# Kernel optimization log

Measured on AMD Instinct MI355X. Metric: run time of the kernel, lower is better.

## Reference

```python
import jax, jax.numpy as jnp
import numpy as np

F = 16      # frames
NV = 4096   # visual points per frame
NT = 512    # tactile points per frame
M = 4096    # model points
SCALE = 0.1


def setup_inputs() -> dict:
    key = jax.random.key(0)
    ks = jax.random.split(key, 6)
    return {
        "state": jax.random.normal(ks[0], (6,), dtype=jnp.float32) * 0.1,
        "model_points": jax.random.normal(ks[1], (M, 3), dtype=jnp.float32),
        "visual_points": jax.random.normal(ks[2], (F, NV, 3), dtype=jnp.float32),
        "tactile_points": jax.random.normal(ks[3], (F, NT, 3), dtype=jnp.float32),
        "physics_pred_states": jax.random.normal(ks[4], (F, 12), dtype=jnp.float32) * 0.1,
        "delta_time": jax.random.uniform(ks[5], (F,), dtype=jnp.float32, minval=0.01, maxval=0.05),
    }


def _skew(a):
    z = jnp.zeros((), a.dtype)
    return jnp.array([[z, -a[2], a[1]],
                      [a[2], z, -a[0]],
                      [-a[1], a[0], z]])


def _rot_from_omega(omega, dt):
    # Rodrigues: R = I + sin(theta*dt) S + (1 - cos(theta*dt)) S@S, S = skew(omega/|omega|)
    theta = jnp.linalg.norm(omega)
    ax = omega / jnp.clip(theta, 1e-8)
    S = _skew(ax)
    return jnp.eye(3, dtype=omega.dtype) + jnp.sin(theta * dt) * S + (1.0 - jnp.cos(theta * dt)) * (S @ S)


def _chamfer(pred, gt):
    # rows: pred [N,3], cols: gt [M,3]; row-min of squared distances, then mean
    d = (jnp.sum(pred * pred, axis=1)[:, None]
         + jnp.sum(gt * gt, axis=1)[None, :]
         - 2.0 * pred @ gt.T)
    return jnp.mean(jnp.min(d, axis=1))


def reference(state, model_points, visual_points, tactile_points, physics_pred_states, delta_time):
    t0 = state[:3]
    r0 = _rot_from_omega(state[3:], jnp.float32(1.0))  # Euler2Mat modeled as axis-angle

    def pose_step(carry, x):
        t, r = carry
        v, omega, dt = x
        t = t + v * dt
        r = _rot_from_omega(omega, dt) @ r
        return (t, r), (t, r)

    _, (ts, rs) = jax.lax.scan(
        pose_step, (t0, r0),
        (physics_pred_states[1:, 6:9], physics_pred_states[1:, 9:12], delta_time[1:]))
    ts = jnp.concatenate([t0[None], ts], axis=0)  # [F,3]
    rs = jnp.concatenate([r0[None], rs], axis=0)  # [F,3,3]

    def frame_loss(acc, x):
        t, r, vp, tp = x
        vc = ((vp - t) @ r) / SCALE
        tc = ((tp - t) @ r) / SCALE
        acc = acc + _chamfer(vc, model_points) + 0.1 * _chamfer(tc, model_points)
        return acc, None

    E_cd, _ = jax.lax.scan(frame_loss, jnp.zeros((), jnp.float32),
                           (ts, rs, visual_points, tactile_points))
    return E_cd
```

## Files before the change

### kernel.cpp

```cpp
#include <hip/hip_runtime.h>
#include <math.h>

#define F_    16
#define NV_   4096
#define NT_   512
#define M_    4096
#define PPF_  (NV_ + NT_)
#define NPTS_ (F_ * PPF_)
#define SCALE_INV 10.0f

#define TPB    256
#define PPT    8
#define PPB    (TPB * PPT)
#define NPB    (NPTS_ / PPB)
#define CHUNK  128
#define NCHUNK (M_ / CHUNK)

__device__ inline void rot_from_omega(float ox, float oy, float oz, float dt,
                                      float* R) {
    float theta = sqrtf(ox * ox + oy * oy + oz * oz);
    float inv = 1.0f / fmaxf(theta, 1e-8f);
    float ax = ox * inv, ay = oy * inv, az = oz * inv;
    float s = sinf(theta * dt);
    float c = 1.0f - cosf(theta * dt);
    R[0] = 1.0f - c * (ay * ay + az * az);
    R[1] = -s * az + c * ax * ay;
    R[2] =  s * ay + c * ax * az;
    R[3] =  s * az + c * ax * ay;
    R[4] = 1.0f - c * (ax * ax + az * az);
    R[5] = -s * ax + c * ay * az;
    R[6] = -s * ax * 0.0f + c * 0.0f;
    R[6] = -s * ay + c * ax * az;
    R[7] =  s * ax + c * ay * az;
    R[8] = 1.0f - c * (ax * ax + ay * ay);
}

__global__ void pose_kernel(const float* __restrict__ state,
                            const float* __restrict__ phys,
                            const float* __restrict__ dts,
                            float* __restrict__ poses,
                            float* __restrict__ out) {
    __shared__ float sRs[F_ * 9];
    __shared__ float sdt[F_ * 3];
    int f = threadIdx.x;
    if (f == 0) out[0] = 0.0f;
    if (f >= 1 && f < F_) {
        float Rs[9];
        float dt = dts[f];
        rot_from_omega(phys[f * 12 + 9], phys[f * 12 + 10], phys[f * 12 + 11], dt, Rs);
        for (int j = 0; j < 9; ++j) sRs[f * 9 + j] = Rs[j];
        sdt[f * 3 + 0] = phys[f * 12 + 6] * dt;
        sdt[f * 3 + 1] = phys[f * 12 + 7] * dt;
        sdt[f * 3 + 2] = phys[f * 12 + 8] * dt;
    }
    __syncthreads();
    if (f == 0) {
        float t[3] = {state[0], state[1], state[2]};
        float R[9];
        rot_from_omega(state[3], state[4], state[5], 1.0f, R);
        for (int i = 0; i < F_; ++i) {
            if (i > 0) {
                t[0] += sdt[i * 3 + 0];
                t[1] += sdt[i * 3 + 1];
                t[2] += sdt[i * 3 + 2];
                float Rn[9];
                const float* Rs = sRs + i * 9;
                for (int r = 0; r < 3; ++r)
                    for (int c2 = 0; c2 < 3; ++c2)
                        Rn[r * 3 + c2] = Rs[r * 3 + 0] * R[0 + c2] +
                                         Rs[r * 3 + 1] * R[3 + c2] +
                                         Rs[r * 3 + 2] * R[6 + c2];
                for (int j = 0; j < 9; ++j) R[j] = Rn[j];
            }
            float* o = poses + i * 12;
            o[0] = t[0]; o[1] = t[1]; o[2] = t[2];
            for (int j = 0; j < 9; ++j) o[3 + j] = R[j] * SCALE_INV;
        }
    }
}

__global__ __launch_bounds__(TPB) void chamfer_main(
    const float* __restrict__ model, const float* __restrict__ vis,
    const float* __restrict__ tac, const float* __restrict__ poses,
    float* __restrict__ partials) {
    __shared__ float4 sfeat[CHUNK];
    __shared__ float sposes[F_ * 12];
    const int pb = blockIdx.x;
    const int ch = blockIdx.y;
    const int mbase = ch * CHUNK;

    if (threadIdx.x < F_ * 12) sposes[threadIdx.x] = poses[threadIdx.x];

    if (threadIdx.x < CHUNK) {
        int i = threadIdx.x;
        float gx = model[(mbase + i) * 3 + 0];
        float gy = model[(mbase + i) * 3 + 1];
        float gz = model[(mbase + i) * 3 + 2];
        sfeat[i] = make_float4(-2.0f * gx, -2.0f * gy, -2.0f * gz,
                               gx * gx + gy * gy + gz * gz);
    }
    __syncthreads();

    float c0[PPT], c1[PPT], c2[PPT], cn[PPT], dm[PPT];
#pragma unroll
    for (int k = 0; k < PPT; ++k) {
        int pt = pb * PPB + k * TPB + threadIdx.x;
        int f = pt / PPF_;
        int loc = pt - f * PPF_;
        const float* p = (loc < NV_) ? (vis + ((size_t)f * NV_ + loc) * 3)
                                     : (tac + ((size_t)f * NT_ + (loc - NV_)) * 3);
        float px = p[0], py = p[1], pz = p[2];
        const float* ps = sposes + f * 12;
        float d0 = px - ps[0], d1 = py - ps[1], d2 = pz - ps[2];
        const float* R = ps + 3;
        float x = d0 * R[0] + d1 * R[3] + d2 * R[6];
        float y = d0 * R[1] + d1 * R[4] + d2 * R[7];
        float z = d0 * R[2] + d1 * R[5] + d2 * R[8];
        c0[k] = x; c1[k] = y; c2[k] = z;
        cn[k] = x * x + y * y + z * z;
        dm[k] = 3.4e38f;
    }

#pragma unroll 4
    for (int m = 0; m < CHUNK; m += 2) {
        float4 ga = sfeat[m];
        float4 gb = sfeat[m + 1];
#pragma unroll
        for (int k = 0; k < PPT; ++k) {
            float da = fmaf(ga.x, c0[k], fmaf(ga.y, c1[k], fmaf(ga.z, c2[k], ga.w)));
            float db = fmaf(gb.x, c0[k], fmaf(gb.y, c1[k], fmaf(gb.z, c2[k], gb.w)));
            dm[k] = fminf(dm[k], fminf(da, db));
        }
    }

#pragma unroll
    for (int k = 0; k < PPT; ++k) {
        int pt = pb * PPB + k * TPB + threadIdx.x;
        partials[(size_t)ch * NPTS_ + pt] = dm[k] + cn[k];
    }
}

__global__ __launch_bounds__(TPB) void chamfer_reduce(
    const float* __restrict__ partials, float* __restrict__ out) {
    int pt = blockIdx.x * TPB + threadIdx.x;
    float m = partials[pt];
    for (int ch = 1; ch < NCHUNK; ++ch)
        m = fminf(m, partials[(size_t)ch * NPTS_ + pt]);
    int loc = pt % PPF_;
    float w = (loc < NV_) ? (1.0f / NV_) : (0.1f / NT_);
    float v = m * w;
#pragma unroll
    for (int off = 32; off > 0; off >>= 1) v += __shfl_down(v, off);
    __shared__ float sw[TPB / 64];
    if ((threadIdx.x & 63) == 0) sw[threadIdx.x >> 6] = v;
    __syncthreads();
    if (threadIdx.x == 0) {
        float s = 0.0f;
        for (int i = 0; i < TPB / 64; ++i) s += sw[i];
        atomicAdd(out, s);
    }
}

#define FB_PPT  2
#define FB_PPB  (TPB * FB_PPT)
#define FB_NPB  (NPTS_ / FB_PPB)

__device__ inline void compute_pose_serial(int f, const float* state,
                                           const float* phys, const float* dts,
                                           float* t, float* R) {
    t[0] = state[0]; t[1] = state[1]; t[2] = state[2];
    rot_from_omega(state[3], state[4], state[5], 1.0f, R);
    for (int i = 1; i <= f; ++i) {
        float dt = dts[i];
        t[0] += phys[i * 12 + 6] * dt;
        t[1] += phys[i * 12 + 7] * dt;
        t[2] += phys[i * 12 + 8] * dt;
        float Rs[9];
        rot_from_omega(phys[i * 12 + 9], phys[i * 12 + 10], phys[i * 12 + 11], dt, Rs);
        float Rn[9];
        for (int r = 0; r < 3; ++r)
            for (int c2 = 0; c2 < 3; ++c2)
                Rn[r * 3 + c2] = Rs[r * 3 + 0] * R[0 + c2] +
                                 Rs[r * 3 + 1] * R[3 + c2] +
                                 Rs[r * 3 + 2] * R[6 + c2];
        for (int j = 0; j < 9; ++j) R[j] = Rn[j];
    }
}

__global__ __launch_bounds__(TPB) void chamfer_fused(
    const float* __restrict__ state, const float* __restrict__ model,
    const float* __restrict__ vis, const float* __restrict__ tac,
    const float* __restrict__ phys, const float* __restrict__ dts,
    float* __restrict__ out) {
    __shared__ float4 sfeat[CHUNK];
    __shared__ float sposes[F_ * 12];
    __shared__ float sw[TPB / 64];

    if (threadIdx.x < F_) {
        float t[3], R[9];
        compute_pose_serial(threadIdx.x, state, phys, dts, t, R);
        float* o = sposes + threadIdx.x * 12;
        o[0] = t[0]; o[1] = t[1]; o[2] = t[2];
        for (int j = 0; j < 9; ++j) o[3 + j] = R[j] * SCALE_INV;
    }
    __syncthreads();

    float c0[FB_PPT], c1[FB_PPT], c2[FB_PPT], cn[FB_PPT], dm[FB_PPT], wt[FB_PPT];
#pragma unroll
    for (int k = 0; k < FB_PPT; ++k) {
        int pt = blockIdx.x * FB_PPB + k * TPB + threadIdx.x;
        int f = pt / PPF_;
        int loc = pt - f * PPF_;
        wt[k] = (loc < NV_) ? (1.0f / NV_) : (0.1f / NT_);
        const float* p = (loc < NV_) ? (vis + ((size_t)f * NV_ + loc) * 3)
                                     : (tac + ((size_t)f * NT_ + (loc - NV_)) * 3);
        float px = p[0], py = p[1], pz = p[2];
        const float* ps = sposes + f * 12;
        float d0 = px - ps[0], d1 = py - ps[1], d2 = pz - ps[2];
        const float* R = ps + 3;
        float x = d0 * R[0] + d1 * R[3] + d2 * R[6];
        float y = d0 * R[1] + d1 * R[4] + d2 * R[7];
        float z = d0 * R[2] + d1 * R[5] + d2 * R[8];
        c0[k] = x; c1[k] = y; c2[k] = z;
        cn[k] = x * x + y * y + z * z;
        dm[k] = 3.4e38f;
    }

    for (int ch = 0; ch < NCHUNK; ++ch) {
        __syncthreads();
        if (threadIdx.x < CHUNK) {
            int i = threadIdx.x;
            int mi = ch * CHUNK + i;
            float gx = model[mi * 3 + 0], gy = model[mi * 3 + 1], gz = model[mi * 3 + 2];
            sfeat[i] = make_float4(-2.0f * gx, -2.0f * gy, -2.0f * gz,
                                   gx * gx + gy * gy + gz * gz);
        }
        __syncthreads();
#pragma unroll 4
        for (int m = 0; m < CHUNK; m += 2) {
            float4 ga = sfeat[m];
            float4 gb = sfeat[m + 1];
#pragma unroll
            for (int k = 0; k < FB_PPT; ++k) {
                float da = fmaf(ga.x, c0[k], fmaf(ga.y, c1[k], fmaf(ga.z, c2[k], ga.w)));
                float db = fmaf(gb.x, c0[k], fmaf(gb.y, c1[k], fmaf(gb.z, c2[k], gb.w)));
                dm[k] = fminf(dm[k], fminf(da, db));
            }
        }
    }

    float v = 0.0f;
#pragma unroll
    for (int k = 0; k < FB_PPT; ++k) v += (dm[k] + cn[k]) * wt[k];
#pragma unroll
    for (int off = 32; off > 0; off >>= 1) v += __shfl_down(v, off);
    if ((threadIdx.x & 63) == 0) sw[threadIdx.x >> 6] = v;
    __syncthreads();
    if (threadIdx.x == 0) {
        float s = 0.0f;
        for (int i = 0; i < TPB / 64; ++i) s += sw[i];
        atomicAdd(out, s);
    }
}

extern "C" void kernel_launch(void* const* d_in, const int* in_sizes, int n_in,
                              void* d_out, int out_size, void* d_ws, size_t ws_size,
                              hipStream_t stream) {
    const float* state = (const float*)d_in[0];
    const float* model = (const float*)d_in[1];
    const float* vis   = (const float*)d_in[2];
    const float* tac   = (const float*)d_in[3];
    const float* phys  = (const float*)d_in[4];
    const float* dts   = (const float*)d_in[5];
    float* out = (float*)d_out;

    const size_t partial_bytes = (size_t)NCHUNK * NPTS_ * sizeof(float);
    const size_t need = partial_bytes + F_ * 12 * sizeof(float);

    if (ws_size >= need) {
        float* partials = (float*)d_ws;
        float* poses = (float*)((char*)d_ws + partial_bytes);
        pose_kernel<<<1, 64, 0, stream>>>(state, phys, dts, poses, out);
        dim3 grid(NPB, NCHUNK);
        chamfer_main<<<grid, TPB, 0, stream>>>(model, vis, tac, poses, partials);
        chamfer_reduce<<<NPTS_ / TPB, TPB, 0, stream>>>(partials, out);
    } else {
        hipMemsetAsync(out, 0, sizeof(float), stream);
        chamfer_fused<<<FB_NPB, TPB, 0, stream>>>(state, model, vis, tac, phys, dts,
                                                  out);
    }
}
```

Before: 103.9 us.

## Fuse pose computation into chamfer kernel and halve model chunk size

Removes the separate single-block pose kernel by having every chamfer block recompute the frame poses into shared memory, which cuts one launch. Reduction now accumulates into a workspace slot and the last block (tracked by a ticket counter) writes the final sum to the output. CHUNK drops from 128 to 64, which doubles the grid's chunk dimension and the size of the partials buffer, so the reduce kernel reads twice as much. The workspace accumulator is zeroed by every main block; this relies on the two kernels running in stream order.

```diff
diff --git a/kernel.cpp b/kernel.cpp
--- a/kernel.cpp
+++ b/kernel.cpp
@@ -13,8 +13,11 @@
 #define PPT    8
 #define PPB    (TPB * PPT)
 #define NPB    (NPTS_ / PPB)
-#define CHUNK  128
+#define CHUNK  64
 #define NCHUNK (M_ / CHUNK)
+#define NRB    (NPTS_ / TPB)
+
+#define WS_PARTIAL_OFF 256
 
 __device__ inline void rot_from_omega(float ox, float oy, float oz, float dt,
                                       float* R) {
@@ -29,35 +32,54 @@
     R[3] =  s * az + c * ax * ay;
     R[4] = 1.0f - c * (ax * ax + az * az);
     R[5] = -s * ax + c * ay * az;
-    R[6] = -s * ax * 0.0f + c * 0.0f;
     R[6] = -s * ay + c * ax * az;
     R[7] =  s * ax + c * ay * az;
     R[8] = 1.0f - c * (ax * ax + ay * ay);
 }
 
-__global__ void pose_kernel(const float* __restrict__ state,
-                            const float* __restrict__ phys,
-                            const float* __restrict__ dts,
-                            float* __restrict__ poses,
-                            float* __restrict__ out) {
+__global__ __launch_bounds__(TPB) void chamfer_main(
+    const float* __restrict__ state, const float* __restrict__ model,
+    const float* __restrict__ vis, const float* __restrict__ tac,
+    const float* __restrict__ phys, const float* __restrict__ dts,
+    float* __restrict__ ws) {
+    __shared__ float4 sfeat[CHUNK];
     __shared__ float sRs[F_ * 9];
     __shared__ float sdt[F_ * 3];
-    int f = threadIdx.x;
-    if (f == 0) out[0] = 0.0f;
-    if (f >= 1 && f < F_) {
+    __shared__ float sposes[F_ * 12];
+    const int tid = threadIdx.x;
+    const int pb = blockIdx.x;
+    const int ch = blockIdx.y;
+    const int mbase = ch * CHUNK;
+    float* __restrict__ partials = ws + (WS_PARTIAL_OFF / 4);
+
+    if (tid < F_) {
         float Rs[9];
-        float dt = dts[f];
-        rot_from_omega(phys[f * 12 + 9], phys[f * 12 + 10], phys[f * 12 + 11], dt, Rs);
-        for (int j = 0; j < 9; ++j) sRs[f * 9 + j] = Rs[j];
-        sdt[f * 3 + 0] = phys[f * 12 + 6] * dt;
-        sdt[f * 3 + 1] = phys[f * 12 + 7] * dt;
-        sdt[f * 3 + 2] = phys[f * 12 + 8] * dt;
-    }
-    __syncthreads();
-    if (f == 0) {
+        if (tid == 0) {
+            rot_from_omega(state[3], state[4], state[5], 1.0f, Rs);
+        } else {
+            float dt = dts[tid];
+            rot_from_omega(phys[tid * 12 + 9], phys[tid * 12 + 10],
+                           phys[tid * 12 + 11], dt, Rs);
+            sdt[tid * 3 + 0] = phys[tid * 12 + 6] * dt;
+            sdt[tid * 3 + 1] = phys[tid * 12 + 7] * dt;
+            sdt[tid * 3 + 2] = phys[tid * 12 + 8] * dt;
+        }
+        for (int j = 0; j < 9; ++j) sRs[tid * 9 + j] = Rs[j];
+    } else if (tid >= 64 && tid < 64 + CHUNK) {
+        int i = tid - 64;
+        float gx = model[(mbase + i) * 3 + 0];
+        float gy = model[(mbase + i) * 3 + 1];
+        float gz = model[(mbase + i) * 3 + 2];
+        sfeat[i] = make_float4(-2.0f * gx, -2.0f * gy, -2.0f * gz,
+                               gx * gx + gy * gy + gz * gz);
+    }
+    if (tid == 32) { ws[0] = 0.0f; ((unsigned*)ws)[1] = 0u; }
+    __syncthreads();
+
+    if (tid == 0) {
         float t[3] = {state[0], state[1], state[2]};
         float R[9];
-        rot_from_omega(state[3], state[4], state[5], 1.0f, R);
+        for (int j = 0; j < 9; ++j) R[j] = sRs[j];
         for (int i = 0; i < F_; ++i) {
             if (i > 0) {
                 t[0] += sdt[i * 3 + 0];
@@ -72,39 +94,17 @@
                                          Rs[r * 3 + 2] * R[6 + c2];
                 for (int j = 0; j < 9; ++j) R[j] = Rn[j];
             }
-            float* o = poses + i * 12;
+            float* o = sposes + i * 12;
             o[0] = t[0]; o[1] = t[1]; o[2] = t[2];
             for (int j = 0; j < 9; ++j) o[3 + j] = R[j] * SCALE_INV;
         }
     }
-}
-
-__global__ __launch_bounds__(TPB) void chamfer_main(
-    const float* __restrict__ model, const float* __restrict__ vis,
-    const float* __restrict__ tac, const float* __restrict__ poses,
-    float* __restrict__ partials) {
-    __shared__ float4 sfeat[CHUNK];
-    __shared__ float sposes[F_ * 12];
-    const int pb = blockIdx.x;
-    const int ch = blockIdx.y;
-    const int mbase = ch * CHUNK;
-
-    if (threadIdx.x < F_ * 12) sposes[threadIdx.x] = poses[threadIdx.x];
-
-    if (threadIdx.x < CHUNK) {
-        int i = threadIdx.x;
-        float gx = model[(mbase + i) * 3 + 0];
-        float gy = model[(mbase + i) * 3 + 1];
-        float gz = model[(mbase + i) * 3 + 2];
-        sfeat[i] = make_float4(-2.0f * gx, -2.0f * gy, -2.0f * gz,
-                               gx * gx + gy * gy + gz * gz);
-    }
     __syncthreads();
 
     float c0[PPT], c1[PPT], c2[PPT], cn[PPT], dm[PPT];
 #pragma unroll
     for (int k = 0; k < PPT; ++k) {
-        int pt = pb * PPB + k * TPB + threadIdx.x;
+        int pt = pb * PPB + k * TPB + tid;
         int f = pt / PPF_;
         int loc = pt - f * PPF_;
         const float* p = (loc < NV_) ? (vis + ((size_t)f * NV_ + loc) * 3)
@@ -135,13 +135,14 @@
 
 #pragma unroll
     for (int k = 0; k < PPT; ++k) {
-        int pt = pb * PPB + k * TPB + threadIdx.x;
+        int pt = pb * PPB + k * TPB + tid;
         partials[(size_t)ch * NPTS_ + pt] = dm[k] + cn[k];
     }
 }
 
 __global__ __launch_bounds__(TPB) void chamfer_reduce(
-    const float* __restrict__ partials, float* __restrict__ out) {
+    float* __restrict__ ws, float* __restrict__ out) {
+    const float* __restrict__ partials = ws + (WS_PARTIAL_OFF / 4);
     int pt = blockIdx.x * TPB + threadIdx.x;
     float m = partials[pt];
     for (int ch = 1; ch < NCHUNK; ++ch)
@@ -157,7 +158,13 @@
     if (threadIdx.x == 0) {
         float s = 0.0f;
         for (int i = 0; i < TPB / 64; ++i) s += sw[i];
-        atomicAdd(out, s);
+        atomicAdd(&ws[0], s);
+        __threadfence();
+        unsigned ticket = atomicAdd(&((unsigned*)ws)[1], 1u);
+        if (ticket == NRB - 1) {
+            float tot = atomicAdd(&ws[0], 0.0f);
+            out[0] = tot;
+        }
     }
 }
 
@@ -274,16 +281,14 @@
     const float* dts   = (const float*)d_in[5];
     float* out = (float*)d_out;
 
-    const size_t partial_bytes = (size_t)NCHUNK * NPTS_ * sizeof(float);
-    const size_t need = partial_bytes + F_ * 12 * sizeof(float);
+    const size_t need = WS_PARTIAL_OFF +
+                        (size_t)NCHUNK * NPTS_ * sizeof(float);
 
     if (ws_size >= need) {
-        float* partials = (float*)d_ws;
-        float* poses = (float*)((char*)d_ws + partial_bytes);
-        pose_kernel<<<1, 64, 0, stream>>>(state, phys, dts, poses, out);
+        float* ws = (float*)d_ws;
         dim3 grid(NPB, NCHUNK);
-        chamfer_main<<<grid, TPB, 0, stream>>>(model, vis, tac, poses, partials);
-        chamfer_reduce<<<NPTS_ / TPB, TPB, 0, stream>>>(partials, out);
+        chamfer_main<<<grid, TPB, 0, stream>>>(state, model, vis, tac, phys, dts, ws);
+        chamfer_reduce<<<NRB, TPB, 0, stream>>>(ws, out);
     } else {
         hipMemsetAsync(out, 0, sizeof(float), stream);
         chamfer_fused<<<FB_NPB, TPB, 0, stream>>>(state, model, vis, tac, phys, dts,
```

Measured after the change: 132.4 us. 27.4% more time.
